# Optimization experiments

Measured on AMD Instinct MI355X. Metric: run time of the kernel, lower is better.

Reference implementation:

```python
import jax, jax.numpy as jnp
import numpy as np

SEQ_LEN = 1024
WINDOW = 32
NUM_HEADS = 16
BATCH = 8
DIM = 1024


def make_local_mask(seq_len=SEQ_LEN, window=WINDOW):
    # True = position is MASKED (disallowed), matching the torch bool attn_mask.
    # torch allows j in [i - window//2, i + window//2] inclusive.
    i = np.arange(seq_len)[:, None]
    j = np.arange(seq_len)[None, :]
    half = window // 2
    allowed = (j >= i - half) & (j <= i + half)
    return jnp.asarray(~allowed)


def setup_inputs() -> dict:
    key = jax.random.key(0)
    k_x, k_wi, k_wo = jax.random.split(key, 3)
    scale_in = 1.0 / np.sqrt(DIM)
    return {
        "x": jax.random.normal(k_x, (BATCH, SEQ_LEN, DIM), dtype=jnp.float32),
        "w_in": jax.random.normal(k_wi, (3 * DIM, DIM), dtype=jnp.float32) * scale_in,
        "b_in": jnp.zeros((3 * DIM,), dtype=jnp.float32),
        "w_out": jax.random.normal(k_wo, (DIM, DIM), dtype=jnp.float32) * scale_in,
        "b_out": jnp.zeros((DIM,), dtype=jnp.float32),
        "mask": make_local_mask(),
    }


def reference(x, w_in, b_in, w_out, b_out, mask):
    B, S, D = x.shape
    H = NUM_HEADS
    hd = D // H
    # fused in-projection (torch nn.MultiheadAttention self-attn path)
    qkv = x @ w_in.T + b_in                      # [B, S, 3D]
    q, k, v = jnp.split(qkv, 3, axis=-1)
    q = q.reshape(B, S, H, hd).transpose(0, 2, 1, 3)  # [B, H, S, hd]
    k = k.reshape(B, S, H, hd).transpose(0, 2, 1, 3)
    v = v.reshape(B, S, H, hd).transpose(0, 2, 1, 3)
    scores = jnp.einsum("bhqd,bhkd->bhqk", q, k) / jnp.sqrt(jnp.asarray(hd, x.dtype))
    neg = jnp.asarray(jnp.finfo(x.dtype).min, x.dtype)
    scores = jnp.where(mask[None, None, :, :], neg, scores)
    attn = jax.nn.softmax(scores, axis=-1)
    ctx = jnp.einsum("bhqk,bhkd->bhqd", attn, v)  # [B, H, S, hd]
    ctx = ctx.transpose(0, 2, 1, 3).reshape(B, S, D)
    return ctx @ w_out.T + b_out
```

## Files before the change

### kernel.cpp

```cpp
#include <hip/hip_runtime.h>

#define S_LEN   1024
#define NH      16
#define HD      64
#define BATCHN  8
#define DMODEL  1024
#define HALF_W  16

typedef __attribute__((ext_vector_type(8))) short bf16x8;
typedef __attribute__((ext_vector_type(4))) float f32x4;

__device__ __forceinline__ unsigned short f2bf(float f) {
  unsigned u = __builtin_bit_cast(unsigned, f);
  u += 0x7fffu + ((u >> 16) & 1u);
  return (unsigned short)(u >> 16);
}
__device__ __forceinline__ float bf2f(unsigned short h) {
  return __builtin_bit_cast(float, ((unsigned)h) << 16);
}

__device__ __forceinline__ void gload_lds16(const void* g, void* l) {
  __builtin_amdgcn_global_load_lds(
      (const __attribute__((address_space(1))) void*)g,
      (__attribute__((address_space(3))) void*)l, 16, 0, 0);
}

__global__ __launch_bounds__(256) void cvt_bf16_kernel(
    const float* __restrict__ in, unsigned short* __restrict__ out, int n4) {
  int t = blockIdx.x * 256 + threadIdx.x;
  if (t >= n4) return;
  float4 v = reinterpret_cast<const float4*>(in)[t];
  ushort4 o = make_ushort4(f2bf(v.x), f2bf(v.y), f2bf(v.z), f2bf(v.w));
  reinterpret_cast<ushort4*>(out)[t] = o;
}

#define MFMA_BF16 __builtin_amdgcn_mfma_f32_16x16x32_bf16

__global__ __launch_bounds__(512, 2) void gemm_inproj_kernel(
    const unsigned short* __restrict__ A,
    const unsigned short* __restrict__ B,
    const float* __restrict__ bias,
    unsigned short* __restrict__ C) {
  __shared__ __align__(16) unsigned short lds[81920];

  const int tid  = threadIdx.x;
  const int lane = tid & 63;
  const int wid  = tid >> 6;
  const int wm   = wid >> 2;
  const int wn   = wid & 3;
  const int lgrp = lane >> 4;
  const int l15  = lane & 15;

  const int sid = (blockIdx.x & 7) * 32 + (blockIdx.x >> 3);
  const int tileM = (sid >> 3) * 256;
  const int tileN = (sid & 7) * 384;

  const int srow = tid >> 2;
  const int scol = ((tid & 3) ^ ((tid >> 3) & 3)) * 8;
  const unsigned short* gA_s = A + (size_t)(tileM + srow) * 1024 + scol;
  const unsigned short* gB_s = B + (size_t)(tileN + srow) * 1024 + scol;

  const int fch  = (lgrp ^ ((l15 >> 1) & 3)) * 8;
  const int arow = (wm * 128 + l15) * 32 + fch;
  const int brow = (wn * 96 + l15) * 32 + fch;

  f32x4 acc[48] = {};

#define STG(S) do { const int _q = (S) & 3;                                \
    const unsigned short* _ga = gA_s + (S) * 32;                           \
    const unsigned short* _gb = gB_s + (S) * 32;                           \
    gload_lds16(_ga,          &lds[_q * 8192 + tid * 8]);                  \
    gload_lds16(_ga + 131072, &lds[_q * 8192 + 4096 + tid * 8]);           \
    gload_lds16(_gb,          &lds[32768 + _q * 12288 + tid * 8]);         \
    gload_lds16(_gb + 131072, &lds[32768 + _q * 12288 + 4096 + tid * 8]);  \
    gload_lds16(_gb + 262144, &lds[32768 + _q * 12288 + 8192 + tid * 8]);  \
  } while (0)

#define M24(MB)                                                            \
    acc[(MB+0)*6+0] = MFMA_BF16(a0_, b0_, acc[(MB+0)*6+0], 0, 0, 0);       \
    acc[(MB+0)*6+1] = MFMA_BF16(a0_, b1_, acc[(MB+0)*6+1], 0, 0, 0);       \
    acc[(MB+0)*6+2] = MFMA_BF16(a0_, b2_, acc[(MB+0)*6+2], 0, 0, 0);       \
    acc[(MB+0)*6+3] = MFMA_BF16(a0_, b3_, acc[(MB+0)*6+3], 0, 0, 0);       \
    acc[(MB+0)*6+4] = MFMA_BF16(a0_, b4_, acc[(MB+0)*6+4], 0, 0, 0);       \
    acc[(MB+0)*6+5] = MFMA_BF16(a0_, b5_, acc[(MB+0)*6+5], 0, 0, 0);       \
    acc[(MB+1)*6+0] = MFMA_BF16(a1_, b0_, acc[(MB+1)*6+0], 0, 0, 0);       \
    acc[(MB+1)*6+1] = MFMA_BF16(a1_, b1_, acc[(MB+1)*6+1], 0, 0, 0);       \
    acc[(MB+1)*6+2] = MFMA_BF16(a1_, b2_, acc[(MB+1)*6+2], 0, 0, 0);       \
    acc[(MB+1)*6+3] = MFMA_BF16(a1_, b3_, acc[(MB+1)*6+3], 0, 0, 0);       \
    acc[(MB+1)*6+4] = MFMA_BF16(a1_, b4_, acc[(MB+1)*6+4], 0, 0, 0);       \
    acc[(MB+1)*6+5] = MFMA_BF16(a1_, b5_, acc[(MB+1)*6+5], 0, 0, 0);       \
    acc[(MB+2)*6+0] = MFMA_BF16(a2_, b0_, acc[(MB+2)*6+0], 0, 0, 0);       \
    acc[(MB+2)*6+1] = MFMA_BF16(a2_, b1_, acc[(MB+2)*6+1], 0, 0, 0);       \
    acc[(MB+2)*6+2] = MFMA_BF16(a2_, b2_, acc[(MB+2)*6+2], 0, 0, 0);       \
    acc[(MB+2)*6+3] = MFMA_BF16(a2_, b3_, acc[(MB+2)*6+3], 0, 0, 0);       \
    acc[(MB+2)*6+4] = MFMA_BF16(a2_, b4_, acc[(MB+2)*6+4], 0, 0, 0);       \
    acc[(MB+2)*6+5] = MFMA_BF16(a2_, b5_, acc[(MB+2)*6+5], 0, 0, 0);       \
    acc[(MB+3)*6+0] = MFMA_BF16(a3_, b0_, acc[(MB+3)*6+0], 0, 0, 0);       \
    acc[(MB+3)*6+1] = MFMA_BF16(a3_, b1_, acc[(MB+3)*6+1], 0, 0, 0);       \
    acc[(MB+3)*6+2] = MFMA_BF16(a3_, b2_, acc[(MB+3)*6+2], 0, 0, 0);       \
    acc[(MB+3)*6+3] = MFMA_BF16(a3_, b3_, acc[(MB+3)*6+3], 0, 0, 0);       \
    acc[(MB+3)*6+4] = MFMA_BF16(a3_, b4_, acc[(MB+3)*6+4], 0, 0, 0);       \
    acc[(MB+3)*6+5] = MFMA_BF16(a3_, b5_, acc[(MB+3)*6+5], 0, 0, 0);

  STG(0); STG(1); STG(2);

#pragma unroll 1
  for (int p = 0; p < 32; ++p) {
    if (p < 30)       { asm volatile("s_waitcnt vmcnt(10)" ::: "memory"); }
    else if (p == 30) { asm volatile("s_waitcnt vmcnt(5)"  ::: "memory"); }
    else              { asm volatile("s_waitcnt vmcnt(0)"  ::: "memory"); }
    __builtin_amdgcn_sched_barrier(0);
    __builtin_amdgcn_s_barrier();

    if (p <= 28) STG(p + 3);

    const int slot = p & 3;
    const unsigned short* pa = &lds[slot * 8192 + arow];
    const unsigned short* pb = &lds[32768 + slot * 12288 + brow];

    bf16x8 b0_ = *(const bf16x8*)(pb);
    bf16x8 b1_ = *(const bf16x8*)(pb + 512);
    bf16x8 b2_ = *(const bf16x8*)(pb + 1024);
    bf16x8 b3_ = *(const bf16x8*)(pb + 1536);
    bf16x8 b4_ = *(const bf16x8*)(pb + 2048);
    bf16x8 b5_ = *(const bf16x8*)(pb + 2560);
    bf16x8 a0_ = *(const bf16x8*)(pa);
    bf16x8 a1_ = *(const bf16x8*)(pa + 512);
    bf16x8 a2_ = *(const bf16x8*)(pa + 1024);
    bf16x8 a3_ = *(const bf16x8*)(pa + 1536);
    asm volatile("s_waitcnt lgkmcnt(0)" ::: "memory");
    __builtin_amdgcn_sched_barrier(0);
    __builtin_amdgcn_s_setprio(1);
    M24(0)
    __builtin_amdgcn_s_setprio(0);

    a0_ = *(const bf16x8*)(pa + 2048);
    a1_ = *(const bf16x8*)(pa + 2560);
    a2_ = *(const bf16x8*)(pa + 3072);
    a3_ = *(const bf16x8*)(pa + 3584);
    asm volatile("s_waitcnt lgkmcnt(0)" ::: "memory");
    __builtin_amdgcn_sched_barrier(0);
    __builtin_amdgcn_s_setprio(1);
    M24(4)
    __builtin_amdgcn_s_setprio(0);
  }
#undef STG
#undef M24

#pragma unroll
  for (int nt = 0; nt < 6; ++nt) {
    const int col = tileN + wn * 96 + nt * 16 + l15;
    const float bs = bias[col];
#pragma unroll
    for (int mt = 0; mt < 8; ++mt) {
      const int row0 = tileM + wm * 128 + mt * 16 + lgrp * 4;
#pragma unroll
      for (int rr = 0; rr < 4; ++rr)
        C[(size_t)(row0 + rr) * 3072 + col] = f2bf(acc[mt * 6 + nt][rr] + bs);
    }
  }
}

__global__ __launch_bounds__(512, 2) void gemm_outproj_kernel(
    const unsigned short* __restrict__ A,
    const unsigned short* __restrict__ B,
    const float* __restrict__ bias,
    float* __restrict__ Cv) {
  __shared__ __align__(16) unsigned short sA[2][2][4096];
  __shared__ __align__(16) unsigned short sB[2][2][8192];

  const int tid  = threadIdx.x;
  const int lane = tid & 63;
  const int wid  = tid >> 6;
  const int wm   = wid >> 2;
  const int wn   = wid & 3;
  const int lgrp = lane >> 4;
  const int l15  = lane & 15;

  const int sid = (blockIdx.x & 7) * 32 + (blockIdx.x >> 3);
  const int tileM = (sid >> 2) * 128;
  const int tileN = (sid & 3) * 256;

  const int srow = tid >> 2;
  const int scol = ((tid & 3) ^ ((tid >> 3) & 3)) * 8;
  const unsigned short* gA_s = A + (size_t)(tileM + srow) * 1024 + scol;
  const unsigned short* gB_s = B + (size_t)(tileN + srow) * 1024 + scol;

  const int fch  = (lgrp ^ ((l15 >> 1) & 3)) * 8;
  const int arow = (wm * 64 + l15) * 32 + fch;
  const int brow = (wn * 64 + l15) * 32 + fch;

  f32x4 acc[4][4] = {};

#define SSA(KT, BUF, KH) do {                                              \
    gload_lds16(gA_s + (KT) * 64 + (KH) * 32, &sA[BUF][KH][wid * 512]);    \
  } while (0)
#define SSB(KT, BUF, KH) do {                                              \
    const unsigned short* _sb = gB_s + (KT) * 64 + (KH) * 32;              \
    gload_lds16(_sb,          &sB[BUF][KH][wid * 512]);                    \
    gload_lds16(_sb + 131072, &sB[BUF][KH][4096 + wid * 512]);             \
  } while (0)

#define GATE(NSTR) do {                                                    \
    asm volatile("s_waitcnt vmcnt(" NSTR ")" ::: "memory");                \
    __builtin_amdgcn_sched_barrier(0);                                     \
    __builtin_amdgcn_s_barrier(); } while (0)

#define PH1(BUF, KH, STGA, STGB) do {                                      \
    STGA; STGB;                                                            \
    const unsigned short* _pa = &sA[BUF][KH][arow];                        \
    const unsigned short* _pb = &sB[BUF][KH][brow];                        \
    bf16x8 a0_ = *(const bf16x8*)(_pa);                                    \
    bf16x8 a1_ = *(const bf16x8*)(_pa + 512);                              \
    bf16x8 a2_ = *(const bf16x8*)(_pa + 1024);                             \
    bf16x8 a3_ = *(const bf16x8*)(_pa + 1536);                             \
    bf16x8 nb0 = *(const bf16x8*)(_pb);                                    \
    bf16x8 nb1 = *(const bf16x8*)(_pb + 512);                              \
    bf16x8 nb2 = *(const bf16x8*)(_pb + 1024);                             \
    bf16x8 nb3 = *(const bf16x8*)(_pb + 1536);                             \
    asm volatile("s_waitcnt lgkmcnt(0)" ::: "memory");                     \
    __builtin_amdgcn_sched_barrier(0);                                     \
    __builtin_amdgcn_s_setprio(1);                                         \
    acc[0][0] = MFMA_BF16(a0_, nb0, acc[0][0], 0, 0, 0);                   \
    acc[0][1] = MFMA_BF16(a0_, nb1, acc[0][1], 0, 0, 0);                   \
    acc[0][2] = MFMA_BF16(a0_, nb2, acc[0][2], 0, 0, 0);                   \
    acc[0][3] = MFMA_BF16(a0_, nb3, acc[0][3], 0, 0, 0);                   \
    acc[1][0] = MFMA_BF16(a1_, nb0, acc[1][0], 0, 0, 0);                   \
    acc[1][1] = MFMA_BF16(a1_, nb1, acc[1][1], 0, 0, 0);                   \
    acc[1][2] = MFMA_BF16(a1_, nb2, acc[1][2], 0, 0, 0);                   \
    acc[1][3] = MFMA_BF16(a1_, nb3, acc[1][3], 0, 0, 0);                   \
    acc[2][0] = MFMA_BF16(a2_, nb0, acc[2][0], 0, 0, 0);                   \
    acc[2][1] = MFMA_BF16(a2_, nb1, acc[2][1], 0, 0, 0);                   \
    acc[2][2] = MFMA_BF16(a2_, nb2, acc[2][2], 0, 0, 0);                   \
    acc[2][3] = MFMA_BF16(a2_, nb3, acc[2][3], 0, 0, 0);                   \
    acc[3][0] = MFMA_BF16(a3_, nb0, acc[3][0], 0, 0, 0);                   \
    acc[3][1] = MFMA_BF16(a3_, nb1, acc[3][1], 0, 0, 0);                   \
    acc[3][2] = MFMA_BF16(a3_, nb2, acc[3][2], 0, 0, 0);                   \
    acc[3][3] = MFMA_BF16(a3_, nb3, acc[3][3], 0, 0, 0);                   \
    __builtin_amdgcn_s_setprio(0);                                         \
  } while (0)
#define NOSTG ((void)0)

  SSA(0, 0, 0); SSB(0, 0, 0);
  SSA(0, 0, 1); SSB(0, 0, 1);
  SSA(1, 1, 0); SSB(1, 1, 0);

#pragma unroll 1
  for (int kt = 0; kt < 14; kt += 2) {
    GATE("6"); PH1(0, 0, SSA(kt + 1, 1, 1), SSB(kt + 1, 1, 1));
    GATE("6"); PH1(0, 1, SSA(kt + 2, 0, 0), SSB(kt + 2, 0, 0));
    GATE("6"); PH1(1, 0, SSA(kt + 2, 0, 1), SSB(kt + 2, 0, 1));
    GATE("6"); PH1(1, 1, SSA(kt + 3, 1, 0), SSB(kt + 3, 1, 0));
  }
  GATE("6"); PH1(0, 0, SSA(15, 1, 1), SSB(15, 1, 1));
  GATE("6"); PH1(0, 1, NOSTG, NOSTG);
  GATE("3"); PH1(1, 0, NOSTG, NOSTG);
  GATE("0"); PH1(1, 1, NOSTG, NOSTG);

#undef SSA
#undef SSB
#undef GATE
#undef PH1
#undef NOSTG

#pragma unroll
  for (int nt = 0; nt < 4; ++nt) {
    const int col = tileN + wn * 64 + nt * 16 + l15;
    const float bs = bias[col];
#pragma unroll
    for (int mt = 0; mt < 4; ++mt) {
      const int row0 = tileM + wm * 64 + mt * 16 + lgrp * 4;
#pragma unroll
      for (int rr = 0; rr < 4; ++rr)
        Cv[(size_t)(row0 + rr) * 1024 + col] = acc[mt][nt][rr] + bs;
    }
  }
}

#define KST 72
#define PST 104

__global__ __launch_bounds__(256) void attn_local_kernel(
    const unsigned short* __restrict__ qkv, unsigned short* __restrict__ ctx) {
  __shared__ __align__(16) unsigned short sKP[96 * KST];
  __shared__ __align__(16) unsigned short sQ[64 * KST];
  __shared__ __align__(16) unsigned short sVT[64 * PST];

  const int tid  = threadIdx.x;
  const int lane = tid & 63;
  const int wid  = tid >> 6;
  const int qc   = lane & 15;
  const int lgrp = lane >> 4;

  const int qb = blockIdx.x & 15;
  const int h  = (blockIdx.x >> 4) & 15;
  const int b  = blockIdx.x >> 8;
  const int i0 = qb * 64;

  const unsigned short* hb = qkv + (size_t)b * S_LEN * 3072 + (size_t)h * HD;

#pragma unroll
  for (int it = 0; it < 3; ++it) {
    int c  = it * 256 + tid;
    int r  = c >> 3;
    int d0 = (c & 7) * 8;
    int j  = i0 - 16 + r;
    bf16x8 kv = {}, vv = {};
    if (0 <= j && j < S_LEN) {
      const unsigned short* rp = hb + (size_t)j * 3072;
      kv = *reinterpret_cast<const bf16x8*>(rp + DMODEL + d0);
      vv = *reinterpret_cast<const bf16x8*>(rp + 2 * DMODEL + d0);
    }
    *reinterpret_cast<bf16x8*>(&sKP[r * KST + d0]) = kv;
#pragma unroll
    for (int jj = 0; jj < 8; ++jj) {
      int dd = (jj + c) & 7;
      sVT[(d0 + dd) * PST + r] = (unsigned short)vv[dd];
    }
  }
#pragma unroll
  for (int it = 0; it < 2; ++it) {
    int c  = it * 256 + tid;
    int r  = c >> 3;
    int d0 = (c & 7) * 8;
    bf16x8 qv = *reinterpret_cast<const bf16x8*>(hb + (size_t)(i0 + r) * 3072 + d0);
    *reinterpret_cast<bf16x8*>(&sQ[r * KST + d0]) = qv;
  }
  __syncthreads();

  const int q0 = wid * 16;

  bf16x8 bq[2];
#pragma unroll
  for (int ks = 0; ks < 2; ++ks)
    bq[ks] = *reinterpret_cast<const bf16x8*>(
        &sQ[(q0 + qc) * KST + ks * 32 + lgrp * 8]);

  f32x4 st[6] = {};
#pragma unroll
  for (int kt = 0; kt < 6; ++kt) {
#pragma unroll
    for (int ks = 0; ks < 2; ++ks) {
      bf16x8 fa = *reinterpret_cast<const bf16x8*>(
          &sKP[(kt * 16 + qc) * KST + ks * 32 + lgrp * 8]);
      st[kt] = __builtin_amdgcn_mfma_f32_16x16x32_bf16(fa, bq[ks], st[kt], 0, 0, 0);
    }
  }
  __syncthreads();

  const int q = q0 + qc;
  float pv[6][4];
  float mx = -3.0e38f;
#pragma unroll
  for (int kt = 0; kt < 6; ++kt)
#pragma unroll
    for (int rr = 0; rr < 4; ++rr) {
      int kk = kt * 16 + lgrp * 4 + rr;
      int j  = i0 - 16 + kk;
      bool ok = (j >= 0) && (j < S_LEN) && (kk >= q) && (kk <= q + 32);
      float s = ok ? st[kt][rr] * 0.125f : -3.0e38f;
      pv[kt][rr] = s;
      mx = fmaxf(mx, s);
    }
  mx = fmaxf(mx, __shfl_xor(mx, 16, 64));
  mx = fmaxf(mx, __shfl_xor(mx, 32, 64));

  float rsum = 0.f;
#pragma unroll
  for (int kt = 0; kt < 6; ++kt)
#pragma unroll
    for (int rr = 0; rr < 4; ++rr) {
      float p = __expf(pv[kt][rr] - mx);
      pv[kt][rr] = p;
      rsum += p;
    }
  rsum += __shfl_xor(rsum, 16, 64);
  rsum += __shfl_xor(rsum, 32, 64);
  const float inv = 1.0f / rsum;

  unsigned short* sP = sKP;
#pragma unroll
  for (int kt = 0; kt < 6; ++kt) {
    ushort4 w = make_ushort4(f2bf(pv[kt][0]), f2bf(pv[kt][1]),
                             f2bf(pv[kt][2]), f2bf(pv[kt][3]));
    *reinterpret_cast<ushort4*>(&sP[(q0 + qc) * PST + kt * 16 + lgrp * 4]) = w;
  }

  bf16x8 pb[3];
#pragma unroll
  for (int ks = 0; ks < 3; ++ks)
    pb[ks] = *reinterpret_cast<const bf16x8*>(
        &sP[(q0 + qc) * PST + ks * 32 + lgrp * 8]);

  f32x4 ct[4] = {};
#pragma unroll
  for (int dt = 0; dt < 4; ++dt)
#pragma unroll
    for (int ks = 0; ks < 3; ++ks) {
      bf16x8 fa = *reinterpret_cast<const bf16x8*>(
          &sVT[(dt * 16 + qc) * PST + ks * 32 + lgrp * 8]);
      ct[dt] = __builtin_amdgcn_mfma_f32_16x16x32_bf16(fa, pb[ks], ct[dt], 0, 0, 0);
    }

  unsigned short* op =
      ctx + ((size_t)b * S_LEN + i0 + q0 + qc) * DMODEL + h * HD;
#pragma unroll
  for (int dt = 0; dt < 4; ++dt) {
    ushort4 w = make_ushort4(
        f2bf(ct[dt][0] * inv), f2bf(ct[dt][1] * inv),
        f2bf(ct[dt][2] * inv), f2bf(ct[dt][3] * inv));
    *reinterpret_cast<ushort4*>(op + dt * 16 + lgrp * 4) = w;
  }
}

extern "C" void kernel_launch(void* const* d_in, const int* in_sizes, int n_in,
                              void* d_out, int out_size, void* d_ws, size_t ws_size,
                              hipStream_t stream) {
  const float* x     = (const float*)d_in[0];
  const float* w_in  = (const float*)d_in[1];
  const float* b_in  = (const float*)d_in[2];
  const float* w_out = (const float*)d_in[3];
  const float* b_out = (const float*)d_in[4];
  float* out = (float*)d_out;

  unsigned short* xb   = (unsigned short*)d_ws;
  unsigned short* wib  = xb  + (size_t)8192 * 1024;
  unsigned short* wob  = wib + (size_t)3072 * 1024;
  unsigned short* qkv  = wob + (size_t)1024 * 1024;
  unsigned short* ctxb = qkv + (size_t)8192 * 3072;

  cvt_bf16_kernel<<<8192, 256, 0, stream>>>(x, xb, (8192 * 1024) / 4);
  cvt_bf16_kernel<<<3072, 256, 0, stream>>>(w_in, wib, (3072 * 1024) / 4);
  cvt_bf16_kernel<<<1024, 256, 0, stream>>>(w_out, wob, (1024 * 1024) / 4);

  gemm_inproj_kernel<<<256, 512, 0, stream>>>(xb, wib, b_in, qkv);

  attn_local_kernel<<<BATCHN * NH * (S_LEN / 64), 256, 0, stream>>>(qkv, ctxb);

  gemm_outproj_kernel<<<256, 512, 0, stream>>>(ctxb, wob, b_out, out);
}
```

Measured before the change: 121.2 us.

## Fuse fp32-to-bf16 conversions into one kernel; triple-buffer out-proj GEMM pipeline

Replaces the three separate bf16 conversion launches with one grid-stride kernel that handles x, w_in and w_out, removing two launches and their tail effects. The out-projection GEMM moves from a double-buffered half-K staging scheme to a 3-slot ring buffer of full 64-wide K tiles, prefetching two tiles ahead with one barrier per K step instead of four. This cuts synchronization and may hide more load latency. In exchange the kernel uses more LDS (144KB), which could limit how many blocks fit per CU despite the occupancy target of 2.

```diff
diff --git a/kernel.cpp b/kernel.cpp
--- a/kernel.cpp
+++ b/kernel.cpp
@@ -25,13 +25,24 @@
       (__attribute__((address_space(3))) void*)l, 16, 0, 0);
 }
 
-__global__ __launch_bounds__(256) void cvt_bf16_kernel(
-    const float* __restrict__ in, unsigned short* __restrict__ out, int n4) {
-  int t = blockIdx.x * 256 + threadIdx.x;
-  if (t >= n4) return;
-  float4 v = reinterpret_cast<const float4*>(in)[t];
-  ushort4 o = make_ushort4(f2bf(v.x), f2bf(v.y), f2bf(v.z), f2bf(v.w));
-  reinterpret_cast<ushort4*>(out)[t] = o;
+#define XT  2097152
+#define WIT  786432
+#define WOT  262144
+__global__ __launch_bounds__(256) void cvt_all_kernel(
+    const float* __restrict__ x, const float* __restrict__ wi,
+    const float* __restrict__ wo,
+    unsigned short* __restrict__ xb, unsigned short* __restrict__ wib,
+    unsigned short* __restrict__ wob) {
+  const int total = XT + WIT + WOT;
+  for (int t = blockIdx.x * 256 + threadIdx.x; t < total; t += 2048 * 256) {
+    const float* in; unsigned short* out; int i;
+    if (t < XT)            { in = x;  out = xb;  i = t; }
+    else if (t < XT + WIT) { in = wi; out = wib; i = t - XT; }
+    else                   { in = wo; out = wob; i = t - XT - WIT; }
+    float4 v = reinterpret_cast<const float4*>(in)[i];
+    ushort4 o = make_ushort4(f2bf(v.x), f2bf(v.y), f2bf(v.z), f2bf(v.w));
+    reinterpret_cast<ushort4*>(out)[i] = o;
+  }
 }
 
 #define MFMA_BF16 __builtin_amdgcn_mfma_f32_16x16x32_bf16
@@ -166,8 +177,7 @@
     const unsigned short* __restrict__ B,
     const float* __restrict__ bias,
     float* __restrict__ Cv) {
-  __shared__ __align__(16) unsigned short sA[2][2][4096];
-  __shared__ __align__(16) unsigned short sB[2][2][8192];
+  __shared__ __align__(16) unsigned short lds[73728];
 
   const int tid  = threadIdx.x;
   const int lane = tid & 63;
@@ -192,24 +202,20 @@
 
   f32x4 acc[4][4] = {};
 
-#define SSA(KT, BUF, KH) do {                                              \
-    gload_lds16(gA_s + (KT) * 64 + (KH) * 32, &sA[BUF][KH][wid * 512]);    \
+#define STG(T) do { const int _q = (T) % 3;                                \
+    const unsigned short* _ga = gA_s + (T) * 64;                           \
+    const unsigned short* _gb = gB_s + (T) * 64;                           \
+    gload_lds16(_ga,               &lds[_q * 24576 + tid * 8]);            \
+    gload_lds16(_ga + 32,          &lds[_q * 24576 + 4096 + tid * 8]);     \
+    gload_lds16(_gb,               &lds[_q * 24576 + 8192 + tid * 8]);     \
+    gload_lds16(_gb + 131072,      &lds[_q * 24576 + 12288 + tid * 8]);    \
+    gload_lds16(_gb + 32,          &lds[_q * 24576 + 16384 + tid * 8]);    \
+    gload_lds16(_gb + 131072 + 32, &lds[_q * 24576 + 20480 + tid * 8]);    \
   } while (0)
-#define SSB(KT, BUF, KH) do {                                              \
-    const unsigned short* _sb = gB_s + (KT) * 64 + (KH) * 32;              \
-    gload_lds16(_sb,          &sB[BUF][KH][wid * 512]);                    \
-    gload_lds16(_sb + 131072, &sB[BUF][KH][4096 + wid * 512]);             \
-  } while (0)
-
-#define GATE(NSTR) do {                                                    \
-    asm volatile("s_waitcnt vmcnt(" NSTR ")" ::: "memory");                \
-    __builtin_amdgcn_sched_barrier(0);                                     \
-    __builtin_amdgcn_s_barrier(); } while (0)
-
-#define PH1(BUF, KH, STGA, STGB) do {                                      \
-    STGA; STGB;                                                            \
-    const unsigned short* _pa = &sA[BUF][KH][arow];                        \
-    const unsigned short* _pb = &sB[BUF][KH][brow];                        \
+
+#define SUB16(KH) do {                                                     \
+    const unsigned short* _pa = &lds[slotb + (KH) * 4096 + arow];          \
+    const unsigned short* _pb = &lds[slotb + 8192 + (KH) * 8192 + brow];   \
     bf16x8 a0_ = *(const bf16x8*)(_pa);                                    \
     bf16x8 a1_ = *(const bf16x8*)(_pa + 512);                              \
     bf16x8 a2_ = *(const bf16x8*)(_pa + 1024);                             \
@@ -239,29 +245,24 @@
     acc[3][3] = MFMA_BF16(a3_, nb3, acc[3][3], 0, 0, 0);                   \
     __builtin_amdgcn_s_setprio(0);                                         \
   } while (0)
-#define NOSTG ((void)0)
-
-  SSA(0, 0, 0); SSB(0, 0, 0);
-  SSA(0, 0, 1); SSB(0, 0, 1);
-  SSA(1, 1, 0); SSB(1, 1, 0);
+
+  STG(0); STG(1);
 
 #pragma unroll 1
-  for (int kt = 0; kt < 14; kt += 2) {
-    GATE("6"); PH1(0, 0, SSA(kt + 1, 1, 1), SSB(kt + 1, 1, 1));
-    GATE("6"); PH1(0, 1, SSA(kt + 2, 0, 0), SSB(kt + 2, 0, 0));
-    GATE("6"); PH1(1, 0, SSA(kt + 2, 0, 1), SSB(kt + 2, 0, 1));
-    GATE("6"); PH1(1, 1, SSA(kt + 3, 1, 0), SSB(kt + 3, 1, 0));
-  }
-  GATE("6"); PH1(0, 0, SSA(15, 1, 1), SSB(15, 1, 1));
-  GATE("6"); PH1(0, 1, NOSTG, NOSTG);
-  GATE("3"); PH1(1, 0, NOSTG, NOSTG);
-  GATE("0"); PH1(1, 1, NOSTG, NOSTG);
-
-#undef SSA
-#undef SSB
-#undef GATE
-#undef PH1
-#undef NOSTG
+  for (int p = 0; p < 16; ++p) {
+    if (p < 15) { asm volatile("s_waitcnt vmcnt(6)" ::: "memory"); }
+    else        { asm volatile("s_waitcnt vmcnt(0)" ::: "memory"); }
+    __builtin_amdgcn_sched_barrier(0);
+    __builtin_amdgcn_s_barrier();
+
+    if (p <= 13) STG(p + 2);
+
+    const int slotb = (p % 3) * 24576;
+    SUB16(0);
+    SUB16(1);
+  }
+#undef STG
+#undef SUB16
 
 #pragma unroll
   for (int nt = 0; nt < 4; ++nt) {
@@ -429,9 +430,7 @@
   unsigned short* qkv  = wob + (size_t)1024 * 1024;
   unsigned short* ctxb = qkv + (size_t)8192 * 3072;
 
-  cvt_bf16_kernel<<<8192, 256, 0, stream>>>(x, xb, (8192 * 1024) / 4);
-  cvt_bf16_kernel<<<3072, 256, 0, stream>>>(w_in, wib, (3072 * 1024) / 4);
-  cvt_bf16_kernel<<<1024, 256, 0, stream>>>(w_out, wob, (1024 * 1024) / 4);
+  cvt_all_kernel<<<2048, 256, 0, stream>>>(x, w_in, w_out, xb, wib, wob);
 
   gemm_inproj_kernel<<<256, 512, 0, stream>>>(xb, wib, b_in, qkv);
 
```

After: 113.3 us, median of 4. -6.5%, faster.
